# Performance work log

Hardware: AMD Instinct MI355X
Metric: run time of the kernel (lower is better)

## Reference

```python
import jax, jax.numpy as jnp
import numpy as np

NEG = -1e30

def setup_inputs() -> dict:
    key = jax.random.key(0)
    k = jax.random.split(key, 6)
    B, Lc, Lq, D = 16, 2048, 256, 256
    c = jax.random.normal(k[0], (B, Lc, D), dtype=jnp.float32)
    q = jax.random.normal(k[1], (B, Lq, D), dtype=jnp.float32)
    c_mask = jnp.ones((B, Lc), dtype=jnp.float32)
    q_mask = jnp.ones((B, Lq), dtype=jnp.float32)
    # xavier-uniform-ish scale for the similarity weights
    lim = float(np.sqrt(6.0 / (D + 1)))
    cq_weight = jax.random.uniform(k[2], (1, 1, D), jnp.float32, -lim, lim)
    c_weight = jax.random.uniform(k[3], (1, D), jnp.float32, -lim, lim)
    q_weight = jax.random.uniform(k[4], (1, D), jnp.float32, -lim, lim)
    bias = jnp.zeros((1,), dtype=jnp.float32)
    return {"c": c, "q": q, "c_mask": c_mask, "q_mask": q_mask,
            "cq_weight": cq_weight, "c_weight": c_weight,
            "q_weight": q_weight, "bias": bias}

def _masked_softmax(logits, mask):
    # mask: 1=keep, 0=pad; broadcast over logits' leading dims
    x = logits * mask + (1.0 - mask) * NEG
    return jax.nn.softmax(x, axis=-1)

def reference(c, q, c_mask, q_mask, cq_weight, c_weight, q_weight, bias):
    # trilinear similarity S[b,i,j] = w_c.c_i + w_q.q_j + (c_i*w_cq).q_j + b
    s0 = jnp.einsum('bid,od->bio', c, c_weight)              # [B,Lc,1]
    s1 = jnp.einsum('bjd,od->boj', q, q_weight)              # [B,1,Lq]
    s2 = jnp.einsum('bid,bjd->bij', c * cq_weight, q)        # [B,Lc,Lq]
    S = s0 + s1 + s2 + bias                                  # [B,Lc,Lq]
    S1 = _masked_softmax(S, q_mask[:, None, :])              # softmax over q
    C2Q = jnp.einsum('bij,bjd->bid', S1, q)                  # [B,Lc,D]
    S2t = _masked_softmax(jnp.swapaxes(S, 1, 2), c_mask[:, None, :])  # [B,Lq,Lc]
    S2 = jnp.einsum('bij,bjk->bik', S1, S2t)                 # [B,Lc,Lc]
    Q2C = jnp.einsum('bik,bkd->bid', S2, c)                  # [B,Lc,D]
    return jnp.concatenate((c, C2Q, c * C2Q, c * Q2C), axis=-1)
```

## Files before the change

### kernel.cpp

```cpp
#include <hip/hip_runtime.h>
#include <hip/hip_bf16.h>

#define NB 16
#define LC 2048
#define LQ 256
#define DD 256
#define NEGINF -1e30f

typedef __attribute__((ext_vector_type(8))) short bf16x8;
typedef __attribute__((ext_vector_type(4))) float f32x4;

#define MFMA16(a, b, c) __builtin_amdgcn_mfma_f32_16x16x32_bf16((a), (b), (c), 0, 0, 0)

typedef const unsigned int __attribute__((address_space(1))) glb_u32;
typedef unsigned int __attribute__((address_space(3))) lds_u32;

__device__ __forceinline__ void gload_lds16(const void* g, void* l) {
    __builtin_amdgcn_global_load_lds((glb_u32*)g, (lds_u32*)l, 16, 0, 0);
}

__device__ __forceinline__ short f2b(float x) {
    unsigned u = __float_as_uint(x);
    unsigned r = (u + 0x7fffu + ((u >> 16) & 1u)) >> 16;
    return (short)r;
}
__device__ __forceinline__ float b2f(short s) {
    return __uint_as_float(((unsigned)(unsigned short)s) << 16);
}

__global__ __launch_bounds__(256) void prep_c(
        const float* __restrict__ c, const float* __restrict__ c_w,
        short* __restrict__ c16, float* __restrict__ s0c) {
    int row = blockIdx.x * 8 + (threadIdx.x >> 5);
    int k = threadIdx.x & 31;
    const float* src = c + (size_t)row * DD + k * 8;
    float4 v0 = *(const float4*)(src);
    float4 v1 = *(const float4*)(src + 4);
    float4 w0 = *(const float4*)(c_w + k * 8);
    float4 w1 = *(const float4*)(c_w + k * 8 + 4);
    float s = v0.x * w0.x + v0.y * w0.y + v0.z * w0.z + v0.w * w0.w
            + v1.x * w1.x + v1.y * w1.y + v1.z * w1.z + v1.w * w1.w;
    #pragma unroll
    for (int o = 16; o > 0; o >>= 1) s += __shfl_xor(s, o, 64);
    if (k == 0) s0c[row] = s;
    ushort4 o0, o1;
    o0.x = (unsigned short)f2b(v0.x); o0.y = (unsigned short)f2b(v0.y);
    o0.z = (unsigned short)f2b(v0.z); o0.w = (unsigned short)f2b(v0.w);
    o1.x = (unsigned short)f2b(v1.x); o1.y = (unsigned short)f2b(v1.y);
    o1.z = (unsigned short)f2b(v1.z); o1.w = (unsigned short)f2b(v1.w);
    ushort4* dst = (ushort4*)(c16 + (size_t)row * DD + k * 8);
    dst[0] = o0;
    dst[1] = o1;
}

__global__ __launch_bounds__(256) void prep_q(
        const float* __restrict__ q, const float* __restrict__ cqw,
        const float* __restrict__ q_w, const float* __restrict__ bias,
        short* __restrict__ qw16, short* __restrict__ qT16,
        float* __restrict__ s1q) {
    __shared__ float T[64][65];
    int b = blockIdx.y, j0 = blockIdx.x * 64, t = threadIdx.x;
    int dd = t & 63, rg = t >> 6;
    float acc[16];
    #pragma unroll
    for (int i = 0; i < 16; ++i) acc[i] = 0.f;
    for (int dc = 0; dc < 4; ++dc) {
        float wv = cqw[dc * 64 + dd];
        float qwv = q_w[dc * 64 + dd];
        #pragma unroll
        for (int rr = 0; rr < 16; ++rr) {
            int r = rg + 4 * rr;
            float v = q[((size_t)b * LQ + j0 + r) * DD + dc * 64 + dd];
            qw16[((size_t)b * LQ + j0 + r) * DD + dc * 64 + dd] = f2b(v * wv);
            acc[rr] += v * qwv;
            T[dd][r] = v;
        }
        __syncthreads();
        int jj = t & 63;
        for (int dw = t >> 6; dw < 64; dw += 4)
            qT16[((size_t)b * DD + dc * 64 + dw) * LQ + j0 + jj] = f2b(T[dw][jj]);
        __syncthreads();
    }
    float bv = bias[0];
    #pragma unroll
    for (int rr = 0; rr < 16; ++rr) {
        float s = acc[rr];
        #pragma unroll
        for (int o = 32; o > 0; o >>= 1) s += __shfl_xor(s, o, 64);
        if (dd == 0) s1q[b * LQ + j0 + rg + 4 * rr] = s + bv;
    }
}

__global__ __launch_bounds__(256) void k1_S(
        const short* __restrict__ c16, const short* __restrict__ qw16,
        const float* __restrict__ cmask,
        const float* __restrict__ s0c, const float* __restrict__ s1q,
        short* __restrict__ Sb, float* __restrict__ pm, float* __restrict__ ps) {
    __shared__ short As[128 * 64];
    __shared__ short Bs[128 * 64];
    int b  = blockIdx.z;
    int i0 = blockIdx.x * 128;
    int j0 = blockIdx.y * 128;
    int t = threadIdx.x;
    int l = t & 63, w = t >> 6;
    int wr = w >> 1, wc = w & 1;

    f32x4 acc[4][4];
    #pragma unroll
    for (int m = 0; m < 4; ++m)
        #pragma unroll
        for (int n = 0; n < 4; ++n) acc[m][n] = (f32x4){0.f, 0.f, 0.f, 0.f};

    const short* Ag = c16  + ((size_t)b * LC + i0) * DD;
    const short* Bg = qw16 + ((size_t)b * LQ + j0) * DD;
    int lrow = l >> 3;
    int lcolsw = ((l & 7) ^ lrow) * 8;

    for (int kt = 0; kt < DD; kt += 64) {
        __syncthreads();
        #pragma unroll
        for (int r = 0; r < 4; ++r) {
            int chunk = r * 4 + w;
            int row = chunk * 8 + lrow;
            gload_lds16(Ag + (size_t)row * DD + kt + lcolsw, As + chunk * 512);
            gload_lds16(Bg + (size_t)row * DD + kt + lcolsw, Bs + chunk * 512);
        }
        __syncthreads();
        #pragma unroll
        for (int kf = 0; kf < 2; ++kf) {
            bf16x8 a[4], bb[4];
            #pragma unroll
            for (int m = 0; m < 4; ++m) {
                int row = wr * 64 + m * 16 + (l & 15);
                int byte = row * 128 + kf * 64 + (l >> 4) * 16;
                a[m] = *(const bf16x8*)((const char*)As + (byte ^ ((row & 7) << 4)));
            }
            #pragma unroll
            for (int n = 0; n < 4; ++n) {
                int row = wc * 64 + n * 16 + (l & 15);
                int byte = row * 128 + kf * 64 + (l >> 4) * 16;
                bb[n] = *(const bf16x8*)((const char*)Bs + (byte ^ ((row & 7) << 4)));
            }
            #pragma unroll
            for (int m = 0; m < 4; ++m)
                #pragma unroll
                for (int n = 0; n < 4; ++n)
                    acc[m][n] = MFMA16(a[m], bb[n], acc[m][n]);
        }
    }

    int jb = j0 + wc * 64;
    float s1v[4];
    #pragma unroll
    for (int n = 0; n < 4; ++n) s1v[n] = s1q[b * LQ + jb + n * 16 + (l & 15)];
    float s0r[4][4], cmr[4][4];
    #pragma unroll
    for (int m = 0; m < 4; ++m)
        #pragma unroll
        for (int reg = 0; reg < 4; ++reg) {
            int il = wr * 64 + m * 16 + (l >> 4) * 4 + reg;
            s0r[m][reg] = s0c[b * LC + i0 + il];
            cmr[m][reg] = cmask[b * LC + i0 + il];
        }
    #pragma unroll
    for (int m = 0; m < 4; ++m)
        #pragma unroll
        for (int n = 0; n < 4; ++n)
            #pragma unroll
            for (int reg = 0; reg < 4; ++reg) {
                float v = acc[m][n][reg] + s0r[m][reg] + s1v[n];
                short sb = f2b(v);
                int il = wr * 64 + m * 16 + (l >> 4) * 4 + reg;
                Sb[((size_t)b * LC + i0 + il) * LQ + jb + n * 16 + (l & 15)] = sb;
                acc[m][n][reg] = b2f(sb);
            }
    #pragma unroll
    for (int n = 0; n < 4; ++n) {
        float x2v[16];
        float mx = NEGINF;
        #pragma unroll
        for (int m = 0; m < 4; ++m)
            #pragma unroll
            for (int reg = 0; reg < 4; ++reg) {
                float cm = cmr[m][reg];
                float x2 = acc[m][n][reg] * cm + (1.f - cm) * NEGINF;
                x2v[m * 4 + reg] = x2;
                mx = fmaxf(mx, x2);
            }
        float ss = 0.f;
        #pragma unroll
        for (int e = 0; e < 16; ++e) ss += __expf(x2v[e] - mx);
        #pragma unroll
        for (int off = 16; off <= 32; off <<= 1) {
            float om = __shfl_xor(mx, off, 64);
            float os = __shfl_xor(ss, off, 64);
            float nm = fmaxf(mx, om);
            ss = ss * __expf(mx - nm) + os * __expf(om - nm);
            mx = nm;
        }
        if (l < 16) {
            size_t idx = ((size_t)b * 32 + blockIdx.x * 2 + wr) * LQ + jb + n * 16 + l;
            pm[idx] = mx;
            ps[idx] = ss;
        }
    }
}

#define K3S 72
__global__ __launch_bounds__(256) void k3_A2C(
        const short* __restrict__ c16, const short* __restrict__ Sb,
        const float* __restrict__ cmask,
        const float* __restrict__ pm, const float* __restrict__ ps,
        float* __restrict__ p3) {
    __shared__ short As[128 * K3S];
    __shared__ short Bs[128 * K3S];
    __shared__ float colCs[128];
    int b  = blockIdx.z;
    int ks = blockIdx.y;
    int d0 = (blockIdx.x >> 1) * 128;
    int j0 = (blockIdx.x & 1) * 128;
    int t = threadIdx.x, l = t & 63, w = t >> 6;
    int wr = w >> 1, wc = w & 1;

    if (t < 128) {
        float m = NEGINF, s = 0.f;
        for (int ch = 0; ch < 32; ++ch) {
            float pmv = pm[((size_t)b * 32 + ch) * LQ + j0 + t];
            float psv = ps[((size_t)b * 32 + ch) * LQ + t + j0];
            float mn = fmaxf(m, pmv);
            s = s * __expf(m - mn) + psv * __expf(pmv - mn);
            m = mn;
        }
        colCs[t] = m + logf(s);
    }
    __syncthreads();

    f32x4 acc[4][4];
    #pragma unroll
    for (int m = 0; m < 4; ++m)
        #pragma unroll
        for (int n = 0; n < 4; ++n) acc[m][n] = (f32x4){0.f, 0.f, 0.f, 0.f};

    int ii = t >> 2;
    int c4 = (t & 3) * 8;

    for (int k0 = ks * 256; k0 < ks * 256 + 256; k0 += 64) {
        __syncthreads();
        float cm = cmask[b * LC + k0 + ii];
        float negc = (1.f - cm) * NEGINF;
        #pragma unroll
        for (int e = 0; e < 4; ++e) {
            int dpos = c4 + e * 32;
            bf16x8 av = *(const bf16x8*)(c16 +
                    ((size_t)(b * LC + k0 + ii)) * DD + d0 + dpos);
            #pragma unroll
            for (int g = 0; g < 8; ++g) As[(dpos + g) * K3S + ii] = av[g];

            int jpos = c4 + e * 32;
            bf16x8 sv8 = *(const bf16x8*)(Sb +
                    ((size_t)(b * LC + k0 + ii)) * LQ + j0 + jpos);
            #pragma unroll
            for (int g = 0; g < 8; ++g) {
                float p = __expf(fmaf(b2f(sv8[g]), cm, negc) - colCs[jpos + g]);
                Bs[(jpos + g) * K3S + ii] = f2b(p);
            }
        }
        __syncthreads();
        #pragma unroll
        for (int kf = 0; kf < 2; ++kf) {
            bf16x8 a[4], bb[4];
            #pragma unroll
            for (int m = 0; m < 4; ++m) {
                int row = wr * 64 + m * 16 + (l & 15);
                a[m] = *(const bf16x8*)((const char*)As +
                        row * (K3S * 2) + kf * 64 + (l >> 4) * 16);
            }
            #pragma unroll
            for (int n = 0; n < 4; ++n) {
                int row = wc * 64 + n * 16 + (l & 15);
                bb[n] = *(const bf16x8*)((const char*)Bs +
                        row * (K3S * 2) + kf * 64 + (l >> 4) * 16);
            }
            #pragma unroll
            for (int m = 0; m < 4; ++m)
                #pragma unroll
                for (int n = 0; n < 4; ++n)
                    acc[m][n] = MFMA16(a[m], bb[n], acc[m][n]);
        }
    }
    float* P = p3 + (((size_t)b * 8 + ks) * 4 + blockIdx.x) * 16384;
    #pragma unroll
    for (int m = 0; m < 4; ++m)
        #pragma unroll
        for (int n = 0; n < 4; ++n)
            #pragma unroll
            for (int reg = 0; reg < 4; ++reg) {
                int ld = wr * 64 + m * 16 + (l >> 4) * 4 + reg;
                int lj = wc * 64 + n * 16 + (l & 15);
                P[ld * 128 + lj] = acc[m][n][reg];
            }
}

__global__ __launch_bounds__(256) void k3r_reduce(
        const float* __restrict__ p3, short* __restrict__ A2CT) {
    int b = blockIdx.y;
    int linear = blockIdx.x * 256 + threadIdx.x;
    int d = linear >> 6;
    int j4 = (linear & 63) * 4;
    int tile = (d >> 7) * 2 + (j4 >> 7);
    int ld = d & 127, lj = j4 & 127;
    const float* base = p3 + (((size_t)b * 8) * 4 + tile) * 16384 + ld * 128 + lj;
    float4 s = {0.f, 0.f, 0.f, 0.f};
    #pragma unroll
    for (int ks = 0; ks < 8; ++ks) {
        float4 v = *(const float4*)(base + (size_t)ks * 4 * 16384);
        s.x += v.x; s.y += v.y; s.z += v.z; s.w += v.w;
    }
    short4 o;
    o.x = f2b(s.x); o.y = f2b(s.y); o.z = f2b(s.z); o.w = f2b(s.w);
    *(short4*)(A2CT + ((size_t)b * DD + d) * LQ + j4) = o;
}

__global__ __launch_bounds__(256) void k4_out(
        const short* __restrict__ Sb, const short* __restrict__ qT16,
        const short* __restrict__ A2CT, const float* __restrict__ c,
        const float* __restrict__ qmask, float* __restrict__ out) {
    __shared__ short P1[64 * 256];
    int b = blockIdx.y, i0 = blockIdx.x * 64;
    int t = threadIdx.x, l = t & 63, w = t >> 6;

    float4 qm4 = *(const float4*)(qmask + b * LQ + l * 4);
    for (int rr = 0; rr < 16; ++rr) {
        int r = rr * 4 + w;
        short4 s4 = *(const short4*)(Sb + ((size_t)b * LC + i0 + r) * LQ + l * 4);
        float x0 = b2f(s4.x) * qm4.x + (1.f - qm4.x) * NEGINF;
        float x1 = b2f(s4.y) * qm4.y + (1.f - qm4.y) * NEGINF;
        float x2 = b2f(s4.z) * qm4.z + (1.f - qm4.z) * NEGINF;
        float x3 = b2f(s4.w) * qm4.w + (1.f - qm4.w) * NEGINF;
        float mx = fmaxf(fmaxf(x0, x1), fmaxf(x2, x3));
        #pragma unroll
        for (int o = 32; o > 0; o >>= 1) mx = fmaxf(mx, __shfl_xor(mx, o, 64));
        float p0 = __expf(x0 - mx), p1 = __expf(x1 - mx);
        float p2 = __expf(x2 - mx), p3v = __expf(x3 - mx);
        float Z = p0 + p1 + p2 + p3v;
        #pragma unroll
        for (int o = 32; o > 0; o >>= 1) Z += __shfl_xor(Z, o, 64);
        float inv = 1.f / Z;
        ushort4 pk;
        pk.x = (unsigned short)f2b(p0 * inv);
        pk.y = (unsigned short)f2b(p1 * inv);
        pk.z = (unsigned short)f2b(p2 * inv);
        pk.w = (unsigned short)f2b(p3v * inv);
        int byte = r * 512 + l * 8;
        *(ushort4*)((char*)P1 + (byte ^ ((r & 7) << 4))) = pk;
    }
    __syncthreads();

    f32x4 acc1[4][4], acc2[4][4];
    #pragma unroll
    for (int m = 0; m < 4; ++m)
        #pragma unroll
        for (int n = 0; n < 4; ++n) {
            acc1[m][n] = (f32x4){0.f, 0.f, 0.f, 0.f};
            acc2[m][n] = (f32x4){0.f, 0.f, 0.f, 0.f};
        }
    const short* qTb = qT16 + (size_t)b * DD * LQ;
    const short* aTb = A2CT + (size_t)b * DD * LQ;
    int d0w = w * 64;
    for (int kf = 0; kf < 8; ++kf) {
        bf16x8 a[4];
        #pragma unroll
        for (int m = 0; m < 4; ++m) {
            int row = m * 16 + (l & 15);
            int byte = row * 512 + kf * 64 + (l >> 4) * 16;
            a[m] = *(const bf16x8*)((const char*)P1 + (byte ^ ((row & 7) << 4)));
        }
        #pragma unroll
        for (int n = 0; n < 4; ++n) {
            int d = d0w + n * 16 + (l & 15);
            size_t off = (size_t)d * LQ + kf * 32 + (l >> 4) * 8;
            bf16x8 bq = *(const bf16x8*)(qTb + off);
            bf16x8 ba = *(const bf16x8*)(aTb + off);
            #pragma unroll
            for (int m = 0; m < 4; ++m) {
                acc1[m][n] = MFMA16(a[m], bq, acc1[m][n]);
                acc2[m][n] = MFMA16(a[m], ba, acc2[m][n]);
            }
        }
    }
    #pragma unroll
    for (int m = 0; m < 4; ++m)
        #pragma unroll
        for (int n = 0; n < 4; ++n)
            #pragma unroll
            for (int reg = 0; reg < 4; ++reg) {
                int i = i0 + m * 16 + (l >> 4) * 4 + reg;
                int d = d0w + n * 16 + (l & 15);
                float cv = c[((size_t)b * LC + i) * DD + d];
                size_t ob = ((size_t)b * LC + i) * (size_t)(4 * DD);
                float v1 = acc1[m][n][reg], v2 = acc2[m][n][reg];
                out[ob + d]           = cv;
                out[ob + 256 + d]     = v1;
                out[ob + 512 + d]     = cv * v1;
                out[ob + 768 + d]     = cv * v2;
            }
}

extern "C" void kernel_launch(void* const* d_in, const int* in_sizes, int n_in,
                              void* d_out, int out_size, void* d_ws, size_t ws_size,
                              hipStream_t stream) {
    const float* c     = (const float*)d_in[0];
    const float* q     = (const float*)d_in[1];
    const float* cmask = (const float*)d_in[2];
    const float* qmask = (const float*)d_in[3];
    const float* cqw   = (const float*)d_in[4];
    const float* c_w   = (const float*)d_in[5];
    const float* q_w   = (const float*)d_in[6];
    const float* bias  = (const float*)d_in[7];
    float* out = (float*)d_out;

    char* w = (char*)d_ws;
    short* Sb    = (short*)(w);
    short* c16   = (short*)(w + 16777216);
    short* qw16  = (short*)(w + 33554432);
    short* qT16  = (short*)(w + 35651584);
    short* A2CT  = (short*)(w + 37748736);
    float* s0c   = (float*)(w + 39845888);
    float* s1q   = (float*)(w + 39976960);
    float* pm    = (float*)(w + 39993344);
    float* ps    = (float*)(w + 40517632);
    float* p3    = (float*)(w + 41041920);

    prep_c<<<dim3(NB * LC / 8), dim3(256), 0, stream>>>(c, c_w, c16, s0c);
    prep_q<<<dim3(LQ / 64, NB), dim3(256), 0, stream>>>(
        q, cqw, q_w, bias, qw16, qT16, s1q);
    k1_S<<<dim3(LC / 128, LQ / 128, NB), dim3(256), 0, stream>>>(
        c16, qw16, cmask, s0c, s1q, Sb, pm, ps);
    k3_A2C<<<dim3(4, 8, NB), dim3(256), 0, stream>>>(
        c16, Sb, cmask, pm, ps, p3);
    k3r_reduce<<<dim3(64, NB), dim3(256), 0, stream>>>(p3, A2CT);
    k4_out<<<dim3(LC / 64, NB), dim3(256), 0, stream>>>(
        Sb, qT16, A2CT, c, qmask, out);
}
```

Before: 129.2 us.

## Compute row softmax log-sum-exp in S kernel and apply it on the fly in output

```diff
diff --git a/kernel.cpp b/kernel.cpp
--- a/kernel.cpp
+++ b/kernel.cpp
@@ -91,19 +91,21 @@
     }
 }
 
-__global__ __launch_bounds__(256) void k1_S(
+__global__ __launch_bounds__(512) void k1_S(
         const short* __restrict__ c16, const short* __restrict__ qw16,
-        const float* __restrict__ cmask,
+        const float* __restrict__ cmask, const float* __restrict__ qmask,
         const float* __restrict__ s0c, const float* __restrict__ s1q,
-        short* __restrict__ Sb, float* __restrict__ pm, float* __restrict__ ps) {
+        short* __restrict__ Sb, float* __restrict__ pm, float* __restrict__ ps,
+        float* __restrict__ rowC) {
     __shared__ short As[128 * 64];
-    __shared__ short Bs[128 * 64];
-    int b  = blockIdx.z;
+    __shared__ short Bs[256 * 64];
+    __shared__ float rmLds[128 * 4];
+    __shared__ float rsLds[128 * 4];
+    int b  = blockIdx.y;
     int i0 = blockIdx.x * 128;
-    int j0 = blockIdx.y * 128;
     int t = threadIdx.x;
     int l = t & 63, w = t >> 6;
-    int wr = w >> 1, wc = w & 1;
+    int wr = w >> 2, wc = w & 3;
 
     f32x4 acc[4][4];
     #pragma unroll
@@ -112,17 +114,22 @@
         for (int n = 0; n < 4; ++n) acc[m][n] = (f32x4){0.f, 0.f, 0.f, 0.f};
 
     const short* Ag = c16  + ((size_t)b * LC + i0) * DD;
-    const short* Bg = qw16 + ((size_t)b * LQ + j0) * DD;
+    const short* Bg = qw16 + ((size_t)b * LQ) * DD;
     int lrow = l >> 3;
     int lcolsw = ((l & 7) ^ lrow) * 8;
 
     for (int kt = 0; kt < DD; kt += 64) {
         __syncthreads();
         #pragma unroll
-        for (int r = 0; r < 4; ++r) {
-            int chunk = r * 4 + w;
+        for (int r = 0; r < 2; ++r) {
+            int chunk = r * 8 + w;
             int row = chunk * 8 + lrow;
             gload_lds16(Ag + (size_t)row * DD + kt + lcolsw, As + chunk * 512);
+        }
+        #pragma unroll
+        for (int r = 0; r < 4; ++r) {
+            int chunk = r * 8 + w;
+            int row = chunk * 8 + lrow;
             gload_lds16(Bg + (size_t)row * DD + kt + lcolsw, Bs + chunk * 512);
         }
         __syncthreads();
@@ -149,10 +156,14 @@
         }
     }
 
-    int jb = j0 + wc * 64;
-    float s1v[4];
-    #pragma unroll
-    for (int n = 0; n < 4; ++n) s1v[n] = s1q[b * LQ + jb + n * 16 + (l & 15)];
+    float s1v[4], qmv[4], negq[4];
+    #pragma unroll
+    for (int n = 0; n < 4; ++n) {
+        int j = wc * 64 + n * 16 + (l & 15);
+        s1v[n] = s1q[b * LQ + j];
+        qmv[n] = qmask[b * LQ + j];
+        negq[n] = (1.f - qmv[n]) * NEGINF;
+    }
     float s0r[4][4], cmr[4][4];
     #pragma unroll
     for (int m = 0; m < 4; ++m)
@@ -171,9 +182,11 @@
                 float v = acc[m][n][reg] + s0r[m][reg] + s1v[n];
                 short sb = f2b(v);
                 int il = wr * 64 + m * 16 + (l >> 4) * 4 + reg;
-                Sb[((size_t)b * LC + i0 + il) * LQ + jb + n * 16 + (l & 15)] = sb;
+                int j = wc * 64 + n * 16 + (l & 15);
+                Sb[((size_t)b * LC + i0 + il) * LQ + j] = sb;
                 acc[m][n][reg] = b2f(sb);
             }
+
     #pragma unroll
     for (int n = 0; n < 4; ++n) {
         float x2v[16];
@@ -199,10 +212,45 @@
             mx = nm;
         }
         if (l < 16) {
-            size_t idx = ((size_t)b * 32 + blockIdx.x * 2 + wr) * LQ + jb + n * 16 + l;
+            int j = wc * 64 + n * 16 + l;
+            size_t idx = ((size_t)b * 32 + blockIdx.x * 2 + wr) * LQ + j;
             pm[idx] = mx;
             ps[idx] = ss;
         }
+    }
+
+    #pragma unroll
+    for (int m = 0; m < 4; ++m)
+        #pragma unroll
+        for (int reg = 0; reg < 4; ++reg) {
+            float mx = NEGINF;
+            #pragma unroll
+            for (int n = 0; n < 4; ++n)
+                mx = fmaxf(mx, fmaf(acc[m][n][reg], qmv[n], negq[n]));
+            #pragma unroll
+            for (int o = 1; o <= 8; o <<= 1) mx = fmaxf(mx, __shfl_xor(mx, o, 64));
+            float ss = 0.f;
+            #pragma unroll
+            for (int n = 0; n < 4; ++n)
+                ss += __expf(fmaf(acc[m][n][reg], qmv[n], negq[n]) - mx);
+            #pragma unroll
+            for (int o = 1; o <= 8; o <<= 1) ss += __shfl_xor(ss, o, 64);
+            if ((l & 15) == 0) {
+                int row = wr * 64 + m * 16 + (l >> 4) * 4 + reg;
+                rmLds[row * 4 + wc] = mx;
+                rsLds[row * 4 + wc] = ss;
+            }
+        }
+    __syncthreads();
+    if (t < 128) {
+        float m0 = rmLds[t * 4 + 0], m1 = rmLds[t * 4 + 1];
+        float m2 = rmLds[t * 4 + 2], m3 = rmLds[t * 4 + 3];
+        float mm = fmaxf(fmaxf(m0, m1), fmaxf(m2, m3));
+        float ss = rsLds[t * 4 + 0] * __expf(m0 - mm)
+                 + rsLds[t * 4 + 1] * __expf(m1 - mm)
+                 + rsLds[t * 4 + 2] * __expf(m2 - mm)
+                 + rsLds[t * 4 + 3] * __expf(m3 - mm);
+        rowC[b * LC + i0 + t] = mm + logf(ss);
     }
 }
 
@@ -244,7 +292,7 @@
     int ii = t >> 2;
     int c4 = (t & 3) * 8;
 
-    for (int k0 = ks * 256; k0 < ks * 256 + 256; k0 += 64) {
+    for (int k0 = ks * 512; k0 < ks * 512 + 512; k0 += 64) {
         __syncthreads();
         float cm = cmask[b * LC + k0 + ii];
         float negc = (1.f - cm) * NEGINF;
@@ -288,7 +336,7 @@
                     acc[m][n] = MFMA16(a[m], bb[n], acc[m][n]);
         }
     }
-    float* P = p3 + (((size_t)b * 8 + ks) * 4 + blockIdx.x) * 16384;
+    float* P = p3 + (((size_t)b * 4 + ks) * 4 + blockIdx.x) * 16384;
     #pragma unroll
     for (int m = 0; m < 4; ++m)
         #pragma unroll
@@ -309,10 +357,10 @@
     int j4 = (linear & 63) * 4;
     int tile = (d >> 7) * 2 + (j4 >> 7);
     int ld = d & 127, lj = j4 & 127;
-    const float* base = p3 + (((size_t)b * 8) * 4 + tile) * 16384 + ld * 128 + lj;
+    const float* base = p3 + (((size_t)b * 4) * 4 + tile) * 16384 + ld * 128 + lj;
     float4 s = {0.f, 0.f, 0.f, 0.f};
     #pragma unroll
-    for (int ks = 0; ks < 8; ++ks) {
+    for (int ks = 0; ks < 4; ++ks) {
         float4 v = *(const float4*)(base + (size_t)ks * 4 * 16384);
         s.x += v.x; s.y += v.y; s.z += v.z; s.w += v.w;
     }
@@ -324,37 +372,16 @@
 __global__ __launch_bounds__(256) void k4_out(
         const short* __restrict__ Sb, const short* __restrict__ qT16,
         const short* __restrict__ A2CT, const float* __restrict__ c,
-        const float* __restrict__ qmask, float* __restrict__ out) {
-    __shared__ short P1[64 * 256];
+        const float* __restrict__ qmask, const float* __restrict__ rowC,
+        float* __restrict__ out) {
     int b = blockIdx.y, i0 = blockIdx.x * 64;
     int t = threadIdx.x, l = t & 63, w = t >> 6;
-
-    float4 qm4 = *(const float4*)(qmask + b * LQ + l * 4);
-    for (int rr = 0; rr < 16; ++rr) {
-        int r = rr * 4 + w;
-        short4 s4 = *(const short4*)(Sb + ((size_t)b * LC + i0 + r) * LQ + l * 4);
-        float x0 = b2f(s4.x) * qm4.x + (1.f - qm4.x) * NEGINF;
-        float x1 = b2f(s4.y) * qm4.y + (1.f - qm4.y) * NEGINF;
-        float x2 = b2f(s4.z) * qm4.z + (1.f - qm4.z) * NEGINF;
-        float x3 = b2f(s4.w) * qm4.w + (1.f - qm4.w) * NEGINF;
-        float mx = fmaxf(fmaxf(x0, x1), fmaxf(x2, x3));
-        #pragma unroll
-        for (int o = 32; o > 0; o >>= 1) mx = fmaxf(mx, __shfl_xor(mx, o, 64));
-        float p0 = __expf(x0 - mx), p1 = __expf(x1 - mx);
-        float p2 = __expf(x2 - mx), p3v = __expf(x3 - mx);
-        float Z = p0 + p1 + p2 + p3v;
-        #pragma unroll
-        for (int o = 32; o > 0; o >>= 1) Z += __shfl_xor(Z, o, 64);
-        float inv = 1.f / Z;
-        ushort4 pk;
-        pk.x = (unsigned short)f2b(p0 * inv);
-        pk.y = (unsigned short)f2b(p1 * inv);
-        pk.z = (unsigned short)f2b(p2 * inv);
-        pk.w = (unsigned short)f2b(p3v * inv);
-        int byte = r * 512 + l * 8;
-        *(ushort4*)((char*)P1 + (byte ^ ((r & 7) << 4))) = pk;
-    }
-    __syncthreads();
+    int d0w = w * 64;
+
+    float rC[4];
+    #pragma unroll
+    for (int m = 0; m < 4; ++m)
+        rC[m] = rowC[b * LC + i0 + m * 16 + (l & 15)];
 
     f32x4 acc1[4][4], acc2[4][4];
     #pragma unroll
@@ -364,21 +391,29 @@
             acc1[m][n] = (f32x4){0.f, 0.f, 0.f, 0.f};
             acc2[m][n] = (f32x4){0.f, 0.f, 0.f, 0.f};
         }
+    const short* Sr  = Sb   + ((size_t)b * LC + i0) * LQ;
     const short* qTb = qT16 + (size_t)b * DD * LQ;
     const short* aTb = A2CT + (size_t)b * DD * LQ;
-    int d0w = w * 64;
+
     for (int kf = 0; kf < 8; ++kf) {
+        int j8 = kf * 32 + (l >> 4) * 8;
+        float4 qa = *(const float4*)(qmask + b * LQ + j8);
+        float4 qb2 = *(const float4*)(qmask + b * LQ + j8 + 4);
+        float qm8[8] = {qa.x, qa.y, qa.z, qa.w, qb2.x, qb2.y, qb2.z, qb2.w};
         bf16x8 a[4];
         #pragma unroll
         for (int m = 0; m < 4; ++m) {
-            int row = m * 16 + (l & 15);
-            int byte = row * 512 + kf * 64 + (l >> 4) * 16;
-            a[m] = *(const bf16x8*)((const char*)P1 + (byte ^ ((row & 7) << 4)));
+            bf16x8 s8 = *(const bf16x8*)(Sr + (size_t)(m * 16 + (l & 15)) * LQ + j8);
+            #pragma unroll
+            for (int g = 0; g < 8; ++g) {
+                float x = fmaf(b2f(s8[g]), qm8[g], (1.f - qm8[g]) * NEGINF) - rC[m];
+                a[m][g] = f2b(__expf(x));
+            }
         }
         #pragma unroll
         for (int n = 0; n < 4; ++n) {
             int d = d0w + n * 16 + (l & 15);
-            size_t off = (size_t)d * LQ + kf * 32 + (l >> 4) * 8;
+            size_t off = (size_t)d * LQ + j8;
             bf16x8 bq = *(const bf16x8*)(qTb + off);
             bf16x8 ba = *(const bf16x8*)(aTb + off);
             #pragma unroll
@@ -430,15 +465,16 @@
     float* pm    = (float*)(w + 39993344);
     float* ps    = (float*)(w + 40517632);
     float* p3    = (float*)(w + 41041920);
+    float* rowC  = (float*)(w + 57819136);
 
     prep_c<<<dim3(NB * LC / 8), dim3(256), 0, stream>>>(c, c_w, c16, s0c);
     prep_q<<<dim3(LQ / 64, NB), dim3(256), 0, stream>>>(
         q, cqw, q_w, bias, qw16, qT16, s1q);
-    k1_S<<<dim3(LC / 128, LQ / 128, NB), dim3(256), 0, stream>>>(
-        c16, qw16, cmask, s0c, s1q, Sb, pm, ps);
-    k3_A2C<<<dim3(4, 8, NB), dim3(256), 0, stream>>>(
+    k1_S<<<dim3(LC / 128, NB), dim3(512), 0, stream>>>(
+        c16, qw16, cmask, qmask, s0c, s1q, Sb, pm, ps, rowC);
+    k3_A2C<<<dim3(4, 4, NB), dim3(256), 0, stream>>>(
         c16, Sb, cmask, pm, ps, p3);
     k3r_reduce<<<dim3(64, NB), dim3(256), 0, stream>>>(p3, A2CT);
     k4_out<<<dim3(LC / 64, NB), dim3(256), 0, stream>>>(
-        Sb, qT16, A2CT, c, qmask, out);
-}
+        Sb, qT16, A2CT, c, qmask, rowC, out);
+}
```

New measurement: 121.0 us. -6.4%, faster.
